# Kernel tuning notes

Measured on AMD Instinct MI355X. Metric: run time of the kernel, lower is better.

## Reference

```python
import jax, jax.numpy as jnp
import numpy as np

B, N, K, DEG = 128, 4096, 25, 16
BN_EPS = 1e-5


def setup_inputs() -> dict:
    key = jax.random.key(0)
    ks = jax.random.split(key, 16)

    def sp_lap(k, V):
        # fixed-degree random sparse scaled Laplacian (COO); values scaled so the
        # K=25 Chebyshev recursion x2 = 2*L@x1 - x0 stays numerically bounded
        rows = jnp.repeat(jnp.arange(V, dtype=jnp.int32), DEG)
        cols = jax.random.randint(k, (V * DEG,), 0, V, dtype=jnp.int32)
        vals = jax.random.normal(jax.random.fold_in(k, 1), (V * DEG,), jnp.float32) * 0.05
        return rows, cols, vals

    l0_rows, l0_cols, l0_vals = sp_lap(ks[0], N)
    l2_rows, l2_cols, l2_vals = sp_lap(ks[1], N // 4)
    l4_rows, l4_cols, l4_vals = sp_lap(ks[2], N // 16)

    x = jax.random.normal(ks[3], (B, N, 1), jnp.float32)
    w1 = jax.random.normal(ks[4], (1 * K, 32), jnp.float32) * 0.1
    b1 = jnp.zeros((32,), jnp.float32)
    w2 = jax.random.normal(ks[5], (32 * K, 64), jnp.float32) * 0.05
    b2 = jnp.zeros((64,), jnp.float32)
    w3 = jax.random.normal(ks[6], (64 * K, 64), jnp.float32) * 0.05
    b3 = jnp.zeros((64,), jnp.float32)
    fc1_w = jax.random.normal(ks[7], (N // 16 * 64, 512), jnp.float32) * 0.01
    fc1_b = jnp.zeros((512,), jnp.float32)
    bn_gamma = jnp.ones((512,), jnp.float32)
    bn_beta = jnp.zeros((512,), jnp.float32)
    fc2_w = jax.random.normal(ks[8], (512, 10), jnp.float32) * 0.05
    fc2_b = jnp.zeros((10,), jnp.float32)

    return dict(x=x,
                l0_rows=l0_rows, l0_cols=l0_cols, l0_vals=l0_vals,
                l2_rows=l2_rows, l2_cols=l2_cols, l2_vals=l2_vals,
                l4_rows=l4_rows, l4_cols=l4_cols, l4_vals=l4_vals,
                w1=w1, b1=b1, w2=w2, b2=b2, w3=w3, b3=b3,
                fc1_w=fc1_w, fc1_b=fc1_b, bn_gamma=bn_gamma, bn_beta=bn_beta,
                fc2_w=fc2_w, fc2_b=fc2_b)


def spmm(rows, cols, vals, xm, V):
    # sparse (V,V) @ dense (V,M) via gather + segment-sum
    return jax.ops.segment_sum(vals[:, None] * xm[cols], rows, num_segments=V)


def cheb(rows, cols, vals, x, W, b):
    # GCNCheb: Chebyshev polynomial basis T_k(L) x, k=0..K-1, then linear projection
    Bb, V, Fin = x.shape
    Kk = W.shape[0] // Fin
    x0 = jnp.transpose(x, (1, 2, 0)).reshape(V, Fin * Bb)  # (V, Fin*B)
    xs = [x0]
    x1 = spmm(rows, cols, vals, x0, V)
    xs.append(x1)
    for _ in range(2, Kk):
        x2 = 2.0 * spmm(rows, cols, vals, x1, V) - x0
        xs.append(x2)
        x0, x1 = x1, x2
    Xc = jnp.stack(xs, 0).reshape(Kk, V, Fin, Bb)          # (K, V, Fin, B)
    Xc = jnp.transpose(Xc, (3, 1, 2, 0)).reshape(Bb * V, Fin * Kk)
    return (Xc @ W + b).reshape(Bb, V, -1)


def pool4(x):
    # max-pool over consecutive groups of 4 nodes (gcn_pool_4)
    Bb, V, F = x.shape
    return x.reshape(Bb, V // 4, 4, F).max(axis=2)


def reference(x,
              l0_rows, l0_cols, l0_vals,
              l2_rows, l2_cols, l2_vals,
              l4_rows, l4_cols, l4_vals,
              w1, b1, w2, b2, w3, b3,
              fc1_w, fc1_b, bn_gamma, bn_beta, fc2_w, fc2_b):
    h = jax.nn.relu(cheb(l0_rows, l0_cols, l0_vals, x, w1, b1))
    h = pool4(h)                                             # (B, N/4, 32)
    h = jax.nn.relu(cheb(l2_rows, l2_cols, l2_vals, h, w2, b2))
    h = pool4(h)                                             # (B, N/16, 64)
    h = jax.nn.relu(cheb(l4_rows, l4_cols, l4_vals, h, w3, b3))
    h = h.reshape(h.shape[0], -1)                            # (B, N/16 * 64)
    h = h @ fc1_w + fc1_b                                    # (B, 512)
    mean = h.mean(axis=0)
    var = h.var(axis=0)  # biased, matching torch BatchNorm training normalization
    h = (h - mean) / jnp.sqrt(var + BN_EPS) * bn_gamma + bn_beta
    h = jax.nn.relu(h)
    logits = h @ fc2_w + fc2_b                               # (B, 10)
    return jax.nn.log_softmax(logits, axis=1)
```

## Files before the change

### kernel.cpp

```cpp
#include <hip/hip_runtime.h>

#define B_ 128
#define K_ 25
#define DEG_ 16

#define R4(X) X(0) X(1) X(2) X(3)

typedef __attribute__((ext_vector_type(4))) float f32x4;
typedef __attribute__((ext_vector_type(8))) short bf16x8;

__device__ __forceinline__ float4 f4ma(float t, float4 w, float4 a) {
    a.x = fmaf(t, w.x, a.x); a.y = fmaf(t, w.y, a.y);
    a.z = fmaf(t, w.z, a.z); a.w = fmaf(t, w.w, a.w);
    return a;
}
__device__ __forceinline__ float4 f4max(float4 a, float4 b) {
    return make_float4(fmaxf(a.x, b.x), fmaxf(a.y, b.y), fmaxf(a.z, b.z), fmaxf(a.w, b.w));
}
__device__ __forceinline__ float4 f4add(float4 a, float4 b) {
    return make_float4(a.x + b.x, a.y + b.y, a.z + b.z, a.w + b.w);
}
__device__ __forceinline__ unsigned f2bfu(float f) {
    unsigned u = __float_as_uint(f);
    return (u + 0x7FFFu + ((u >> 16) & 1u)) >> 16;
}
__device__ __forceinline__ unsigned packbf(float e, float o) { return f2bfu(e) | (f2bfu(o) << 16); }

__device__ __forceinline__ bf16x8 u2b(uint4 u) {
    union { uint4 u4; bf16x8 b8; } c; c.u4 = u; return c.b8;
}
__device__ __forceinline__ f32x4 mfma_bf(uint4 a, uint4 b, f32x4 c) {
    return __builtin_amdgcn_mfma_f32_16x16x32_bf16(u2b(a), u2b(b), c, 0, 0, 0);
}

__global__ __launch_bounds__(256) void k_transpose_x(const float* __restrict__ x, float* __restrict__ x0) {
    int i = blockIdx.x * 256 + threadIdx.x;
    int v = i >> 7, b = i & 127;
    x0[i] = x[(b << 12) + v];
}

__global__ __launch_bounds__(256) void k_packw(const float* __restrict__ w2, const float* __restrict__ w3,
        unsigned short* __restrict__ wb2, unsigned short* __restrict__ wb3) {
    int i = blockIdx.x * 256 + threadIdx.x;
    if (i < 51200) {
        int k = i >> 11, rem = i & 2047, fo = rem >> 5, fi = rem & 31;
        wb2[i] = (unsigned short)f2bfu(w2[(size_t)(fi * K_ + k) * 64 + fo]);
    }
    if (i < 102400) {
        int k = i >> 12, rem = i & 4095, fo = rem >> 6, fi = rem & 63;
        wb3[i] = (unsigned short)f2bfu(w3[(size_t)(fi * K_ + k) * 64 + fo]);
    }
}

__global__ __launch_bounds__(256) void k_spmm1(const int* __restrict__ cols, const float* __restrict__ vals,
        const float4* __restrict__ cur, const float4* __restrict__ prev,
        float4* __restrict__ next, int two) {
    int t = blockIdx.x * 256 + threadIdx.x;
    int v = t >> 5, lane = t & 31;
    int base = v * DEG_;
    float4 s0 = make_float4(0.f, 0.f, 0.f, 0.f), s1 = s0;
#pragma unroll
    for (int d = 0; d < 8; ++d) {
        s0 = f4ma(vals[base + d],     cur[((size_t)cols[base + d] << 5) + lane], s0);
        s1 = f4ma(vals[base + 8 + d], cur[((size_t)cols[base + 8 + d] << 5) + lane], s1);
    }
    float4 s = f4add(s0, s1);
    size_t idx = ((size_t)v << 5) + lane;
    if (two) {
        float4 p = prev[idx];
        s.x = 2.f * s.x - p.x; s.y = 2.f * s.y - p.y;
        s.z = 2.f * s.z - p.z; s.w = 2.f * s.w - p.w;
    }
    next[idx] = s;
}

template<int LOGC4>
__global__ __launch_bounds__(256) void k_spmm4(const int* __restrict__ cols, const float* __restrict__ vals,
                        const float4* __restrict__ cur, const float4* __restrict__ prev,
                        float4* __restrict__ next, unsigned* __restrict__ mir, int two) {
    constexpr int LOGW4 = LOGC4 - 3;
    int xcd = blockIdx.x & 7, q = blockIdx.x >> 3;
    int tid = q * 256 + threadIdx.x;
    int v = __builtin_amdgcn_readfirstlane(tid >> LOGW4);
    int c4 = (xcd << LOGW4) + (tid & ((1 << LOGW4) - 1));
    int base = v * DEG_;
    float4 s0 = make_float4(0.f, 0.f, 0.f, 0.f), s1 = s0, s2 = s0, s3 = s0;
#pragma unroll
    for (int d = 0; d < 4; ++d) {
        s0 = f4ma(vals[base + d],      cur[((size_t)cols[base + d] << LOGC4) + c4], s0);
        s1 = f4ma(vals[base + 4 + d],  cur[((size_t)cols[base + 4 + d] << LOGC4) + c4], s1);
        s2 = f4ma(vals[base + 8 + d],  cur[((size_t)cols[base + 8 + d] << LOGC4) + c4], s2);
        s3 = f4ma(vals[base + 12 + d], cur[((size_t)cols[base + 12 + d] << LOGC4) + c4], s3);
    }
    float4 s = f4add(f4add(s0, s1), f4add(s2, s3));
    size_t idx = ((size_t)v << LOGC4) + c4;
    if (two) {
        float4 p = prev[idx];
        s.x = 2.f * s.x - p.x; s.y = 2.f * s.y - p.y;
        s.z = 2.f * s.z - p.z; s.w = 2.f * s.w - p.w;
    }
    next[idx] = s;
    float tx = __shfl_down(s.x, 32), ty = __shfl_down(s.y, 32),
          tz = __shfl_down(s.z, 32), tw = __shfl_down(s.w, 32);
    if ((threadIdx.x & 63) < 32) {
        int c = c4 << 2;
        int fi2 = c >> 8, b0 = c & 127;
        uint4 m = make_uint4(packbf(s.x, tx), packbf(s.y, ty), packbf(s.z, tz), packbf(s.w, tw));
        *(uint4*)(mir + ((size_t)v << (LOGC4 + 1)) + ((size_t)fi2 << 7) + b0) = m;
    }
}

__global__ __launch_bounds__(256) void k_proj1_pool(const float* __restrict__ basis,
        const float* __restrict__ W1, const float* __restrict__ b1, float* __restrict__ pool1,
        unsigned* __restrict__ mir) {
    int half = blockIdx.y;
    int i = blockIdx.x * 256 + threadIdx.x;
    int g = i >> 7, b = i & 127;
    const float* wbase = W1 + half * 16;
#define P1_DM(j) float4 M##j = make_float4(-1e30f, -1e30f, -1e30f, -1e30f);
    R4(P1_DM)
#undef P1_DM
    for (int r = 0; r < 4; ++r) {
        const float* bp = basis + (((size_t)(4 * g + r) << 7) + b);
#define P1_DC(j) float4 C##j = make_float4(0.f, 0.f, 0.f, 0.f);
        R4(P1_DC)
#undef P1_DC
#pragma unroll 5
        for (int k = 0; k < K_; ++k) {
            float tv = bp[(size_t)k * 524288];
            const float4* w = (const float4*)(wbase + k * 32);
#define P1_FM(j) C##j = f4ma(tv, w[j], C##j);
            R4(P1_FM)
#undef P1_FM
        }
#define P1_MX(j) M##j = f4max(M##j, C##j);
        R4(P1_MX)
#undef P1_MX
    }
    float* op = pool1 + ((size_t)g << 12) + ((size_t)half << 11) + b;
    unsigned* mp = mir + ((size_t)g << 11) + ((size_t)half << 10) + b;
    const float* bb = b1 + half * 16;
#define P1_ST(j) { \
    float e0 = fmaxf(M##j.x + bb[4*j+0], 0.f); \
    float o0 = fmaxf(M##j.y + bb[4*j+1], 0.f); \
    float e1 = fmaxf(M##j.z + bb[4*j+2], 0.f); \
    float o1 = fmaxf(M##j.w + bb[4*j+3], 0.f); \
    op[(4*j+0)*128] = e0; op[(4*j+1)*128] = o0; \
    op[(4*j+2)*128] = e1; op[(4*j+3)*128] = o1; \
    mp[(2*j+0)*128] = packbf(e0, o0); \
    mp[(2*j+1)*128] = packbf(e1, o1); }
    R4(P1_ST)
#undef P1_ST
}

__global__ __launch_bounds__(256) void k_proj_l2m(const unsigned* __restrict__ mir, size_t slotH,
        const uint4* __restrict__ wb, float* __restrict__ acc, int k0, int init,
        const float* __restrict__ bias) {
    int wid = blockIdx.x * 4 + (threadIdx.x >> 6);
    int lane = threadIdx.x & 63;
    int lm = lane & 15, lg = lane >> 4;
    int v = wid >> 3, b0 = (wid & 7) << 4;
    float* ap = acc + ((size_t)v << 13) + b0 + (lg << 2);
    f32x4 C0, C1, C2, C3;
    if (init) {
        float q0 = bias[lm], q1 = bias[16 + lm], q2 = bias[32 + lm], q3 = bias[48 + lm];
        C0 = f32x4{q0, q0, q0, q0}; C1 = f32x4{q1, q1, q1, q1};
        C2 = f32x4{q2, q2, q2, q2}; C3 = f32x4{q3, q3, q3, q3};
    } else {
        C0 = *(const f32x4*)(ap + (size_t)lm * 128);
        C1 = *(const f32x4*)(ap + (size_t)(16 + lm) * 128);
        C2 = *(const f32x4*)(ap + (size_t)(32 + lm) * 128);
        C3 = *(const f32x4*)(ap + (size_t)(48 + lm) * 128);
    }
    const unsigned* mp0 = mir + ((size_t)v << 11) + (lg << 9) + b0 + lm;
#pragma unroll
    for (int kk = 0; kk < 5; ++kk) {
        const unsigned* mp = mp0 + (size_t)kk * slotH;
        uint4 a = make_uint4(mp[0], mp[128], mp[256], mp[384]);
        int kb = (k0 + kk) << 6;
        uint4 w0 = wb[(kb + lm) * 4 + lg];
        uint4 w1 = wb[(kb + 16 + lm) * 4 + lg];
        uint4 w2 = wb[(kb + 32 + lm) * 4 + lg];
        uint4 w3 = wb[(kb + 48 + lm) * 4 + lg];
        C0 = mfma_bf(a, w0, C0);
        C1 = mfma_bf(a, w1, C1);
        C2 = mfma_bf(a, w2, C2);
        C3 = mfma_bf(a, w3, C3);
    }
    *(f32x4*)(ap + (size_t)lm * 128) = C0;
    *(f32x4*)(ap + (size_t)(16 + lm) * 128) = C1;
    *(f32x4*)(ap + (size_t)(32 + lm) * 128) = C2;
    *(f32x4*)(ap + (size_t)(48 + lm) * 128) = C3;
}

__global__ __launch_bounds__(256) void k_proj_l3m(const unsigned* __restrict__ mir, size_t slotH,
        const uint4* __restrict__ wb, float* __restrict__ acc, int k0, int init,
        const float* __restrict__ bias, int finalrelu) {
    int wid = blockIdx.x * 4 + (threadIdx.x >> 6);
    int lane = threadIdx.x & 63;
    int lm = lane & 15, lg = lane >> 4;
    int v = wid >> 3, b0 = (wid & 7) << 4;
    float* ap = acc + ((size_t)v << 13) + b0 + (lg << 2);
    f32x4 C0, C1, C2, C3;
    if (init) {
        float q0 = bias[lm], q1 = bias[16 + lm], q2 = bias[32 + lm], q3 = bias[48 + lm];
        C0 = f32x4{q0, q0, q0, q0}; C1 = f32x4{q1, q1, q1, q1};
        C2 = f32x4{q2, q2, q2, q2}; C3 = f32x4{q3, q3, q3, q3};
    } else {
        C0 = *(const f32x4*)(ap + (size_t)lm * 128);
        C1 = *(const f32x4*)(ap + (size_t)(16 + lm) * 128);
        C2 = *(const f32x4*)(ap + (size_t)(32 + lm) * 128);
        C3 = *(const f32x4*)(ap + (size_t)(48 + lm) * 128);
    }
    const unsigned* mp0 = mir + ((size_t)v << 12) + b0 + lm;
#pragma unroll
    for (int kk = 0; kk < 5; ++kk) {
        const unsigned* mp = mp0 + (size_t)kk * slotH;
        int kb = (k0 + kk) << 6;
#pragma unroll
        for (int ks = 0; ks < 2; ++ks) {
            const unsigned* mk = mp + (size_t)((ks << 4) + (lg << 2)) * 128;
            uint4 a = make_uint4(mk[0], mk[128], mk[256], mk[384]);
            int wof = (ks << 2) + lg;
            uint4 w0 = wb[(kb + lm) * 8 + wof];
            uint4 w1 = wb[(kb + 16 + lm) * 8 + wof];
            uint4 w2 = wb[(kb + 32 + lm) * 8 + wof];
            uint4 w3 = wb[(kb + 48 + lm) * 8 + wof];
            C0 = mfma_bf(a, w0, C0);
            C1 = mfma_bf(a, w1, C1);
            C2 = mfma_bf(a, w2, C2);
            C3 = mfma_bf(a, w3, C3);
        }
    }
    if (finalrelu) {
#pragma unroll
        for (int r = 0; r < 4; ++r) {
            C0[r] = fmaxf(C0[r], 0.f); C1[r] = fmaxf(C1[r], 0.f);
            C2[r] = fmaxf(C2[r], 0.f); C3[r] = fmaxf(C3[r], 0.f);
        }
    }
    *(f32x4*)(ap + (size_t)lm * 128) = C0;
    *(f32x4*)(ap + (size_t)(16 + lm) * 128) = C1;
    *(f32x4*)(ap + (size_t)(32 + lm) * 128) = C2;
    *(f32x4*)(ap + (size_t)(48 + lm) * 128) = C3;
}

__global__ __launch_bounds__(256) void k_relu_pool_m(const float* __restrict__ acc,
        float* __restrict__ pool, unsigned* __restrict__ mir) {
    int i = blockIdx.x * 256 + threadIdx.x;
    int g = i >> 12, fi2 = (i >> 7) & 31, b = i & 127;
    const float* ap = acc + (((size_t)g << 2) << 13) + (fi2 << 8) + b;
    float me = 0.f, mo = 0.f;
#pragma unroll
    for (int r = 0; r < 4; ++r) {
        me = fmaxf(me, ap[0]); mo = fmaxf(mo, ap[128]);
        ap += 8192;
    }
    size_t po = ((size_t)g << 13) + (fi2 << 8) + b;
    pool[po] = me; pool[po + 128] = mo;
    mir[i] = packbf(me, mo);
}

__global__ __launch_bounds__(256) void k_fc1_part(const float* __restrict__ t3, const float* __restrict__ w,
                           float* __restrict__ part) {
    int blk = blockIdx.x;
    int bg = blk >> 7;
    int rs = (blk >> 1) & 63;
    int j = ((blk & 1) << 8) + threadIdx.x;
    int b0 = bg << 3;
    float a0=0.f,a1=0.f,a2=0.f,a3=0.f,a4=0.f,a5=0.f,a6=0.f,a7=0.f;
    int r0 = rs << 8;
#pragma unroll 4
    for (int row = r0; row < r0 + 256; ++row) {
        float wv = w[((size_t)row << 9) + j];
        const float4* tp = (const float4*)(t3 + ((size_t)row << 7) + b0);
        float4 t0 = tp[0], t1 = tp[1];
        a0 = fmaf(t0.x, wv, a0);
        a1 = fmaf(t0.y, wv, a1);
        a2 = fmaf(t0.z, wv, a2);
        a3 = fmaf(t0.w, wv, a3);
        a4 = fmaf(t1.x, wv, a4);
        a5 = fmaf(t1.y, wv, a5);
        a6 = fmaf(t1.z, wv, a6);
        a7 = fmaf(t1.w, wv, a7);
    }
    float* pp = part + (((size_t)(rs << 7) + b0) << 9) + j;
    pp[0*512]=a0; pp[1*512]=a1; pp[2*512]=a2; pp[3*512]=a3;
    pp[4*512]=a4; pp[5*512]=a5; pp[6*512]=a6; pp[7*512]=a7;
}

__global__ __launch_bounds__(256) void k_fc1_red(const float* __restrict__ part, const float* __restrict__ bias,
                          float* __restrict__ h) {
    int i = blockIdx.x * 256 + threadIdx.x;
    float a = bias[i & 511];
#pragma unroll 8
    for (int rs = 0; rs < 64; ++rs) a += part[((size_t)rs << 16) + i];
    h[i] = a;
}

__global__ void k_bnstats(const float* __restrict__ h, float* __restrict__ mv) {
    __shared__ float s1[128], s2[128];
    int j = blockIdx.x, t = threadIdx.x;
    float v = h[(size_t)t * 512 + j];
    s1[t] = v; s2[t] = v * v;
    __syncthreads();
    for (int o = 64; o > 0; o >>= 1) {
        if (t < o) { s1[t] += s1[t + o]; s2[t] += s2[t + o]; }
        __syncthreads();
    }
    if (t == 0) {
        float m = s1[0] * (1.f / 128.f);
        float var = s2[0] * (1.f / 128.f) - m * m;
        mv[j] = m;
        mv[512 + j] = rsqrtf(var + 1e-5f);
    }
}

__global__ void k_head(const float* __restrict__ h, const float* __restrict__ mv,
                       const float* __restrict__ gamma, const float* __restrict__ beta,
                       const float* __restrict__ w2, const float* __restrict__ b2,
                       float* __restrict__ out) {
    __shared__ float hr[512];
    __shared__ float lg[16];
    int b = blockIdx.x, t = threadIdx.x;
    for (int j = t; j < 512; j += 64) {
        float x = (h[(size_t)b * 512 + j] - mv[j]) * mv[512 + j] * gamma[j] + beta[j];
        hr[j] = fmaxf(x, 0.f);
    }
    __syncthreads();
    if (t < 10) {
        float a = b2[t];
        for (int j = 0; j < 512; ++j) a += hr[j] * w2[j * 10 + t];
        lg[t] = a;
    }
    __syncthreads();
    if (t == 0) {
        float mx = -1e30f;
        for (int q = 0; q < 10; ++q) mx = fmaxf(mx, lg[q]);
        float sum = 0.f;
        for (int q = 0; q < 10; ++q) sum += expf(lg[q] - mx);
        float ls = logf(sum) + mx;
        for (int q = 0; q < 10; ++q) out[b * 10 + q] = lg[q] - ls;
    }
}

extern "C" void kernel_launch(void* const* d_in, const int* in_sizes, int n_in,
                              void* d_out, int out_size, void* d_ws, size_t ws_size,
                              hipStream_t stream) {
    (void)in_sizes; (void)n_in; (void)out_size; (void)ws_size;
    const float* x      = (const float*)d_in[0];
    const int*   l0cols = (const int*)d_in[2];
    const float* l0vals = (const float*)d_in[3];
    const int*   l2cols = (const int*)d_in[5];
    const float* l2vals = (const float*)d_in[6];
    const int*   l4cols = (const int*)d_in[8];
    const float* l4vals = (const float*)d_in[9];
    const float* w1   = (const float*)d_in[10];
    const float* b1   = (const float*)d_in[11];
    const float* w2   = (const float*)d_in[12];
    const float* b2   = (const float*)d_in[13];
    const float* w3   = (const float*)d_in[14];
    const float* b3   = (const float*)d_in[15];
    const float* fc1w = (const float*)d_in[16];
    const float* fc1b = (const float*)d_in[17];
    const float* gam  = (const float*)d_in[18];
    const float* bet  = (const float*)d_in[19];
    const float* fc2w = (const float*)d_in[20];
    const float* fc2b = (const float*)d_in[21];
    float* out = (float*)d_out;

    const size_t S1 = 4096 * 128;
    const size_t S2 = 1024 * 4096;
    const size_t S3 = 256 * 8192;
    const int CKP = 5;

    float* ws = (float*)d_ws;
    float* basis1 = ws;
    float* ring2f = ws + 25 * S1;
    unsigned* mir2 = (unsigned*)(ring2f + 3 * S2);
    float* tailp  = (float*)(mir2 + (size_t)CKP * (S2 / 2));
    float* h      = tailp;
    float* mv     = h + 65536;
    unsigned short* wb2 = (unsigned short*)(mv + 1024);
    unsigned short* wb3 = wb2 + 51200;
    float* acc2   = basis1;
    float* ring3f = ring2f;
    float* acc3   = ring2f + 3 * S3;
    unsigned* mir3 = mir2;
    float* part   = basis1;

    k_packw<<<400, 256, 0, stream>>>(w2, w3, wb2, wb3);

    k_transpose_x<<<2048, 256, 0, stream>>>(x, basis1);
    for (int k = 1; k < 25; ++k) {
        const float* cur  = basis1 + (size_t)(k - 1) * S1;
        const float* prev = (k >= 2) ? basis1 + (size_t)(k - 2) * S1 : cur;
        float* next = basis1 + (size_t)k * S1;
        k_spmm1<<<512, 256, 0, stream>>>(l0cols, l0vals, (const float4*)cur,
                                         (const float4*)prev, (float4*)next, k >= 2 ? 1 : 0);
    }
    k_proj1_pool<<<dim3(512, 2), 256, 0, stream>>>(basis1, w1, b1, ring2f, mir2);

    {
        int cs = 0;
        for (int k = 0; k < 25; ++k) {
            if (k >= 1) {
                const float* cur  = ring2f + (size_t)((k - 1) % 3) * S2;
                const float* prev = ring2f + (size_t)((k >= 2 ? k - 2 : 0) % 3) * S2;
                float* next = ring2f + (size_t)(k % 3) * S2;
                unsigned* mirp = mir2 + (size_t)(k % CKP) * (S2 / 2);
                k_spmm4<10><<<4096, 256, 0, stream>>>(l2cols, l2vals, (const float4*)cur,
                                                      (const float4*)prev, (float4*)next,
                                                      mirp, k >= 2 ? 1 : 0);
            }
            if (k - cs + 1 == CKP) {
                k_proj_l2m<<<2048, 256, 0, stream>>>(mir2, S2 / 2, (const uint4*)wb2, acc2, cs,
                                                     cs == 0 ? 1 : 0, b2);
                cs = k + 1;
            }
        }
    }
    k_relu_pool_m<<<4096, 256, 0, stream>>>(acc2, ring3f , mir3 );

    {
        int cs = 0;
        for (int k = 0; k < 25; ++k) {
            if (k >= 1) {
                const float* cur  = ring3f + (size_t)((k - 1) % 3) * S3;
                const float* prev = ring3f + (size_t)((k >= 2 ? k - 2 : 0) % 3) * S3;
                float* next = ring3f + (size_t)(k % 3) * S3;
                unsigned* mirp = mir3 + (size_t)(k % CKP) * (S3 / 2);
                k_spmm4<11><<<2048, 256, 0, stream>>>(l4cols, l4vals, (const float4*)cur,
                                                      (const float4*)prev, (float4*)next,
                                                      mirp, k >= 2 ? 1 : 0);
            }
            if (k - cs + 1 == CKP) {
                k_proj_l3m<<<512, 256, 0, stream>>>(mir3, S3 / 2, (const uint4*)wb3, acc3, cs,
                                                    cs == 0 ? 1 : 0, b3, cs == 20 ? 1 : 0);
                cs = k + 1;
            }
        }
    }

    k_fc1_part<<<2048, 256, 0, stream>>>(acc3, fc1w, part);
    k_fc1_red<<<256, 256, 0, stream>>>(part, fc1b, h);
    k_bnstats<<<512, 128, 0, stream>>>(h, mv);
    k_head<<<128, 64, 0, stream>>>(h, mv, gam, bet, fc2w, fc2b, out);
}
```

Before: 919.7 us.

## Gather SpMM inputs from the bf16 mirror instead of the fp32 Chebyshev state

The layer-2 and layer-3 Chebyshev SpMM kernels now gather neighbour rows from the packed bf16 mirror written by the previous step, unpacking even and odd batch halves, instead of from fp32 state. fp32 state is kept only for the 2*Lx - x_prev term. That state is cut to a two-buffer ping-pong updated in place, and each thread now handles 8 values. The goal is to halve the bytes moved by the random-access gathers, which dominate these bandwidth-bound kernels. The cost is that bf16 rounding error now enters the 25-step recursion itself, not only the projection inputs, which could hurt accuracy.

```diff
diff --git a/kernel.cpp b/kernel.cpp
--- a/kernel.cpp
+++ b/kernel.cpp
@@ -20,11 +20,22 @@
 __device__ __forceinline__ float4 f4add(float4 a, float4 b) {
     return make_float4(a.x + b.x, a.y + b.y, a.z + b.z, a.w + b.w);
 }
+__device__ __forceinline__ float4 f4sub2(float4 s, float4 p) {
+    return make_float4(2.f * s.x - p.x, 2.f * s.y - p.y, 2.f * s.z - p.z, 2.f * s.w - p.w);
+}
 __device__ __forceinline__ unsigned f2bfu(float f) {
     unsigned u = __float_as_uint(f);
     return (u + 0x7FFFu + ((u >> 16) & 1u)) >> 16;
 }
 __device__ __forceinline__ unsigned packbf(float e, float o) { return f2bfu(e) | (f2bfu(o) << 16); }
+__device__ __forceinline__ float4 mevens(uint4 m) {
+    return make_float4(__uint_as_float(m.x << 16), __uint_as_float(m.y << 16),
+                       __uint_as_float(m.z << 16), __uint_as_float(m.w << 16));
+}
+__device__ __forceinline__ float4 modds(uint4 m) {
+    return make_float4(__uint_as_float(m.x & 0xFFFF0000u), __uint_as_float(m.y & 0xFFFF0000u),
+                       __uint_as_float(m.z & 0xFFFF0000u), __uint_as_float(m.w & 0xFFFF0000u));
+}
 
 __device__ __forceinline__ bf16x8 u2b(uint4 u) {
     union { uint4 u4; bf16x8 b8; } c; c.u4 = u; return c.b8;
@@ -74,40 +85,43 @@
     next[idx] = s;
 }
 
-template<int LOGC4>
-__global__ __launch_bounds__(256) void k_spmm4(const int* __restrict__ cols, const float* __restrict__ vals,
-                        const float4* __restrict__ cur, const float4* __restrict__ prev,
-                        float4* __restrict__ next, unsigned* __restrict__ mir, int two) {
-    constexpr int LOGW4 = LOGC4 - 3;
+template<int LOGF2>
+__global__ __launch_bounds__(256) void k_spmm4m(const int* __restrict__ cols, const float* __restrict__ vals,
+        const unsigned* __restrict__ mirPrev, float* __restrict__ st,
+        unsigned* __restrict__ mirOut, int two) {
+    constexpr int SL = LOGF2 + 2;
+    constexpr int MSTR = 1 << (LOGF2 + 7);
     int xcd = blockIdx.x & 7, q = blockIdx.x >> 3;
-    int tid = q * 256 + threadIdx.x;
-    int v = __builtin_amdgcn_readfirstlane(tid >> LOGW4);
-    int c4 = (xcd << LOGW4) + (tid & ((1 << LOGW4) - 1));
+    int v = __builtin_amdgcn_readfirstlane((q << (8 - SL)) + (threadIdx.x >> SL));
+    int l = threadIdx.x & ((1 << SL) - 1);
+    int cc = (xcd << SL) + l;
+    int fi2 = cc >> 5, b0 = (cc & 31) << 2;
     int base = v * DEG_;
-    float4 s0 = make_float4(0.f, 0.f, 0.f, 0.f), s1 = s0, s2 = s0, s3 = s0;
-#pragma unroll
-    for (int d = 0; d < 4; ++d) {
-        s0 = f4ma(vals[base + d],      cur[((size_t)cols[base + d] << LOGC4) + c4], s0);
-        s1 = f4ma(vals[base + 4 + d],  cur[((size_t)cols[base + 4 + d] << LOGC4) + c4], s1);
-        s2 = f4ma(vals[base + 8 + d],  cur[((size_t)cols[base + 8 + d] << LOGC4) + c4], s2);
-        s3 = f4ma(vals[base + 12 + d], cur[((size_t)cols[base + 12 + d] << LOGC4) + c4], s3);
-    }
-    float4 s = f4add(f4add(s0, s1), f4add(s2, s3));
-    size_t idx = ((size_t)v << LOGC4) + c4;
+    int moff = (fi2 << 7) + b0;
+    float4 eA = make_float4(0.f, 0.f, 0.f, 0.f), eB = eA, oA = eA, oB = eA;
+#pragma unroll
+    for (int d = 0; d < 8; ++d) {
+        {
+            float w = vals[base + d];
+            uint4 m = *(const uint4*)(mirPrev + (size_t)cols[base + d] * MSTR + moff);
+            eA = f4ma(w, mevens(m), eA); oA = f4ma(w, modds(m), oA);
+        }
+        {
+            float w = vals[base + 8 + d];
+            uint4 m = *(const uint4*)(mirPrev + (size_t)cols[base + 8 + d] * MSTR + moff);
+            eB = f4ma(w, mevens(m), eB); oB = f4ma(w, modds(m), oB);
+        }
+    }
+    float4 e = f4add(eA, eB), o = f4add(oA, oB);
+    size_t sidx = ((size_t)v << (LOGF2 + 8)) + (fi2 << 8) + b0;
     if (two) {
-        float4 p = prev[idx];
-        s.x = 2.f * s.x - p.x; s.y = 2.f * s.y - p.y;
-        s.z = 2.f * s.z - p.z; s.w = 2.f * s.w - p.w;
-    }
-    next[idx] = s;
-    float tx = __shfl_down(s.x, 32), ty = __shfl_down(s.y, 32),
-          tz = __shfl_down(s.z, 32), tw = __shfl_down(s.w, 32);
-    if ((threadIdx.x & 63) < 32) {
-        int c = c4 << 2;
-        int fi2 = c >> 8, b0 = c & 127;
-        uint4 m = make_uint4(packbf(s.x, tx), packbf(s.y, ty), packbf(s.z, tz), packbf(s.w, tw));
-        *(uint4*)(mir + ((size_t)v << (LOGC4 + 1)) + ((size_t)fi2 << 7) + b0) = m;
-    }
+        float4 pe = *(const float4*)(st + sidx), po = *(const float4*)(st + sidx + 128);
+        e = f4sub2(e, pe); o = f4sub2(o, po);
+    }
+    *(float4*)(st + sidx) = e;
+    *(float4*)(st + sidx + 128) = o;
+    *(uint4*)(mirOut + (size_t)v * MSTR + moff) =
+        make_uint4(packbf(e.x, o.x), packbf(e.y, o.y), packbf(e.z, o.z), packbf(e.w, o.w));
 }
 
 __global__ __launch_bounds__(256) void k_proj1_pool(const float* __restrict__ basis,
@@ -372,20 +386,21 @@
     const size_t S1 = 4096 * 128;
     const size_t S2 = 1024 * 4096;
     const size_t S3 = 256 * 8192;
-    const int CKP = 5;
 
     float* ws = (float*)d_ws;
     float* basis1 = ws;
-    float* ring2f = ws + 25 * S1;
-    unsigned* mir2 = (unsigned*)(ring2f + 3 * S2);
-    float* tailp  = (float*)(mir2 + (size_t)CKP * (S2 / 2));
+    float* st2A   = ws + 25 * S1;
+    float* st2B   = st2A + S2;
+    unsigned* mir2 = (unsigned*)(st2B + S2);
+    float* tailp  = (float*)(mir2 + 5 * (S2 / 2));
     float* h      = tailp;
     float* mv     = h + 65536;
     unsigned short* wb2 = (unsigned short*)(mv + 1024);
     unsigned short* wb3 = wb2 + 51200;
     float* acc2   = basis1;
-    float* ring3f = ring2f;
-    float* acc3   = ring2f + 3 * S3;
+    float* st3A   = st2A;
+    float* st3B   = st2A + S3;
+    float* acc3   = st2B;
     unsigned* mir3 = mir2;
     float* part   = basis1;
 
@@ -399,42 +414,36 @@
         k_spmm1<<<512, 256, 0, stream>>>(l0cols, l0vals, (const float4*)cur,
                                          (const float4*)prev, (float4*)next, k >= 2 ? 1 : 0);
     }
-    k_proj1_pool<<<dim3(512, 2), 256, 0, stream>>>(basis1, w1, b1, ring2f, mir2);
+    k_proj1_pool<<<dim3(512, 2), 256, 0, stream>>>(basis1, w1, b1, st2A, mir2);
 
     {
+        float* s2[2] = {st2A, st2B};
         int cs = 0;
         for (int k = 0; k < 25; ++k) {
             if (k >= 1) {
-                const float* cur  = ring2f + (size_t)((k - 1) % 3) * S2;
-                const float* prev = ring2f + (size_t)((k >= 2 ? k - 2 : 0) % 3) * S2;
-                float* next = ring2f + (size_t)(k % 3) * S2;
-                unsigned* mirp = mir2 + (size_t)(k % CKP) * (S2 / 2);
-                k_spmm4<10><<<4096, 256, 0, stream>>>(l2cols, l2vals, (const float4*)cur,
-                                                      (const float4*)prev, (float4*)next,
-                                                      mirp, k >= 2 ? 1 : 0);
+                k_spmm4m<4><<<2048, 256, 0, stream>>>(l2cols, l2vals,
+                    mir2 + (size_t)((k - 1) % 5) * (S2 / 2), s2[k & 1],
+                    mir2 + (size_t)(k % 5) * (S2 / 2), k >= 2 ? 1 : 0);
             }
-            if (k - cs + 1 == CKP) {
+            if (k - cs + 1 == 5) {
                 k_proj_l2m<<<2048, 256, 0, stream>>>(mir2, S2 / 2, (const uint4*)wb2, acc2, cs,
                                                      cs == 0 ? 1 : 0, b2);
                 cs = k + 1;
             }
         }
     }
-    k_relu_pool_m<<<4096, 256, 0, stream>>>(acc2, ring3f , mir3 );
+    k_relu_pool_m<<<4096, 256, 0, stream>>>(acc2, st3A , mir3 );
 
     {
+        float* s3[2] = {st3A, st3B};
         int cs = 0;
         for (int k = 0; k < 25; ++k) {
             if (k >= 1) {
-                const float* cur  = ring3f + (size_t)((k - 1) % 3) * S3;
-                const float* prev = ring3f + (size_t)((k >= 2 ? k - 2 : 0) % 3) * S3;
-                float* next = ring3f + (size_t)(k % 3) * S3;
-                unsigned* mirp = mir3 + (size_t)(k % CKP) * (S3 / 2);
-                k_spmm4<11><<<2048, 256, 0, stream>>>(l4cols, l4vals, (const float4*)cur,
-                                                      (const float4*)prev, (float4*)next,
-                                                      mirp, k >= 2 ? 1 : 0);
+                k_spmm4m<5><<<1024, 256, 0, stream>>>(l4cols, l4vals,
+                    mir3 + (size_t)((k - 1) % 5) * (S3 / 2), s3[k & 1],
+                    mir3 + (size_t)(k % 5) * (S3 / 2), k >= 2 ? 1 : 0);
             }
-            if (k - cs + 1 == CKP) {
+            if (k - cs + 1 == 5) {
                 k_proj_l3m<<<512, 256, 0, stream>>>(mir3, S3 / 2, (const uint4*)wb3, acc3, cs,
                                                     cs == 0 ? 1 : 0, b3, cs == 20 ? 1 : 0);
                 cs = k + 1;
```

Result: faster. 808.2 us (-12.1%).
